# Performance work log

Measured on AMD Instinct MI355X. Metric: run time of the kernel, lower is better.

## Reference

```python
import jax, jax.numpy as jnp
import numpy as np

B, T, D = 1, 1024, 4096
H, HK, DH = 32, 8, 128          # n_heads, n_kv_heads, head_dim
N_REP = H // HK                 # GQA repeat factor
RQ, RKV, RO, RFF = 64, 64, 1024, 1024
INTER = 14336
EPS = 1e-5
THETA = 10000.0


def _rms_norm(x, w):
    # LLaMA RMSNorm: x * rsqrt(mean(x^2)+eps) * w
    var = jnp.mean(x * x, axis=-1, keepdims=True)
    return x * jax.lax.rsqrt(var + EPS) * w


def _rope_cos_sin(t_len, dh):
    # _SimpleRoPE semantics: interleaved repeat of angles (repeat_interleave(2))
    evens = jnp.arange(0, dh, 2, dtype=jnp.float32)
    inv = 1.0 / (THETA ** (evens / dh))                 # [dh/2]
    t = jnp.arange(t_len, dtype=jnp.float32)
    ang = t[:, None] * inv[None, :]                     # [T, dh/2]
    ang = jnp.repeat(ang, 2, axis=-1)                   # [T, dh]
    return jnp.cos(ang), jnp.sin(ang)


def _rotate_half(x):
    # HF rotate_half: split in half along last dim
    half = x.shape[-1] // 2
    return jnp.concatenate([-x[..., half:], x[..., :half]], axis=-1)


def _apply_rope(q, k, cos, sin):
    # q,k: [B,H,T,dh]; cos/sin: [T,dh] broadcast over B,H
    c = cos[None, None]
    s = sin[None, None]
    return q * c + _rotate_half(q) * s, k * c + _rotate_half(k) * s


def _proj_per_head(x, Us, V):
    # x: [B,T,D], V: [h,r,D], Us: [h,dh,r] -> [B,h,T,dh]
    xr = jnp.einsum('btd,hrd->bthr', x, V)
    return jnp.einsum('bthr,hdr->bhtd', xr, Us)


def setup_inputs() -> dict:
    key = jax.random.key(0)
    ks = jax.random.split(key, 16)
    sc = 0.02
    inp = {
        'hidden_states': jax.random.normal(ks[0], (B, T, D), jnp.float32),
        'ln1_w': jnp.ones((D,), jnp.float32),
        'ln2_w': jnp.ones((D,), jnp.float32),
        'q_Us': jax.random.normal(ks[1], (H, DH, RQ), jnp.float32) * sc,
        'q_V': jax.random.normal(ks[2], (H, RQ, D), jnp.float32) * sc,
        'k_Us': jax.random.normal(ks[3], (HK, DH, RKV), jnp.float32) * sc,
        'k_V': jax.random.normal(ks[4], (HK, RKV, D), jnp.float32) * sc,
        'v_Us': jax.random.normal(ks[5], (HK, DH, RKV), jnp.float32) * sc,
        'v_V': jax.random.normal(ks[6], (HK, RKV, D), jnp.float32) * sc,
        'o_Us': jax.random.normal(ks[7], (D, RO), jnp.float32) * sc,
        'o_V': jax.random.normal(ks[8], (RO, H * DH), jnp.float32) * sc,
        'g_Us': jax.random.normal(ks[9], (INTER, RFF), jnp.float32) * sc,
        'g_V': jax.random.normal(ks[10], (RFF, D), jnp.float32) * sc,
        'u_Us': jax.random.normal(ks[11], (INTER, RFF), jnp.float32) * sc,
        'u_V': jax.random.normal(ks[12], (RFF, D), jnp.float32) * sc,
        'd_Us': jax.random.normal(ks[13], (D, RFF), jnp.float32) * sc,
        'd_V': jax.random.normal(ks[14], (RFF, INTER), jnp.float32) * sc,
    }
    return inp


def reference(hidden_states, ln1_w, ln2_w, q_Us, q_V, k_Us, k_V, v_Us, v_V,
              o_Us, o_V, g_Us, g_V, u_Us, u_V, d_Us, d_V):
    x = hidden_states
    # --- attention ---
    h1 = _rms_norm(x, ln1_w)
    q = _proj_per_head(h1, q_Us, q_V)            # [B,H,T,dh]
    k = _proj_per_head(h1, k_Us, k_V)            # [B,HK,T,dh]
    v = _proj_per_head(h1, v_Us, v_V)            # [B,HK,T,dh]
    cos, sin = _rope_cos_sin(T, DH)
    q, k = _apply_rope(q, k, cos, sin)
    k = jnp.repeat(k, N_REP, axis=1)             # GQA expand -> [B,H,T,dh]
    v = jnp.repeat(v, N_REP, axis=1)
    scale = 1.0 / np.sqrt(DH)
    scores = jnp.einsum('bhtd,bhsd->bhts', q, k) * scale   # [B,H,T,T]
    causal = jnp.tril(jnp.ones((T, T), bool))
    scores = jnp.where(causal[None, None], scores, jnp.float32(-1e30))
    p = jax.nn.softmax(scores, axis=-1)
    attn = jnp.einsum('bhts,bhsd->bhtd', p, v)   # [B,H,T,dh]
    attn = attn.transpose(0, 2, 1, 3).reshape(B, T, H * DH)
    # low-rank o: y = attn @ W_o^T = (attn @ V^T) @ Us^T
    y = jnp.einsum('btr,dr->btd', jnp.einsum('bte,re->btr', attn, o_V), o_Us)
    x = x + y
    # --- SwiGLU MLP with low-rank factors ---
    h2 = _rms_norm(x, ln2_w)
    g = jnp.einsum('btr,ir->bti', jnp.einsum('btd,rd->btr', h2, g_V), g_Us)
    u = jnp.einsum('btr,ir->bti', jnp.einsum('btd,rd->btr', h2, u_V), u_Us)
    hmid = jax.nn.silu(g) * u                    # [B,T,INTER]
    dn = jnp.einsum('btr,dr->btd', jnp.einsum('bti,ri->btr', hmid, d_V), d_Us)
    return x + dn
```

## Files before the change

kernel.cpp:

```cpp
#include <hip/hip_runtime.h>
#include <math.h>


typedef __bf16 bf16;
typedef __bf16 bf16x8 __attribute__((ext_vector_type(8)));
typedef __bf16 bf16x4 __attribute__((ext_vector_type(4)));
typedef float  f32x4  __attribute__((ext_vector_type(4)));

#define EPI_BF16   0
#define EPI_BF16T  1
#define EPI_F32ADD 2
#define EPI_SILU1  3
#define EPI_MUL    4
#define EPI_PART   5

__device__ __forceinline__ void gld16(const void* g, void* l) {
    __builtin_amdgcn_global_load_lds(
        (const __attribute__((address_space(1))) unsigned int*)g,
        (__attribute__((address_space(3))) unsigned int*)l, 16, 0, 0);
}

template<int EPI>
__global__ __launch_bounds__(256)
void gemm3(const bf16* __restrict__ A, int lda, long sA,
           const bf16* __restrict__ B, int ldb, long sB, const bf16* __restrict__ B2,
           void* __restrict__ Cv, int ldc, long sC,
           const float* __restrict__ R, int Kc, int nsplit, int gx)
{
    __shared__ __align__(16) bf16 As[128 * 64];
    __shared__ __align__(16) bf16 Bs[128 * 64];

    const int tid = threadIdx.x, lane = tid & 63, w = tid >> 6;
    const int wr = w >> 1, wc = w & 1;

    int id = blockIdx.x;
    {
        const int nwg = gridDim.x;
        int q = nwg >> 3, rr = nwg & 7;
        int xcd = id & 7, off = id >> 3;
        id = (xcd < rr ? xcd * (q + 1) : rr * (q + 1) + (xcd - rr) * q) + off;
    }
    const int bm = id % gx, bn = id / gx, bz = blockIdx.z;
    const int ks = bz % nsplit, zb = bz / nsplit;

    const bf16* Bp = (B2 != nullptr && zb != 0) ? B2 : B;
    const bf16* Ab = A  + (long)zb * sA + (long)(bm * 128) * lda + (long)ks * Kc;
    const bf16* Bb = Bp + (long)zb * sB + (long)(bn * 128) * ldb + (long)ks * Kc;

    const int g = lane >> 4, r = lane & 15;
    f32x4 acc[4][4] = {};
    const int nt = Kc >> 6;

    for (int t = 0; t < nt; t++) {
        if (t) __syncthreads();
        const bf16* At = Ab + t * 64;
        const bf16* Bt = Bb + t * 64;
        #pragma unroll
        for (int i = 0; i < 4; i++) {
            int cb = w * 256 + i * 64, ci = cb + lane;
            int row = ci >> 3, col = ((ci & 7) ^ (row & 7)) * 8;
            gld16(At + (long)row * lda + col, &As[cb * 8]);
            gld16(Bt + (long)row * ldb + col, &Bs[cb * 8]);
        }
        __syncthreads();
        #pragma unroll
        for (int kk = 0; kk < 2; kk++) {
            bf16x8 af[4], bfr[4];
            #pragma unroll
            for (int m = 0; m < 4; m++) {
                int row = wr * 64 + m * 16 + r;
                af[m] = *(const bf16x8*)&As[row * 64 + (((kk * 4 + g) ^ (row & 7)) * 8)];
            }
            #pragma unroll
            for (int n = 0; n < 4; n++) {
                int row = wc * 64 + n * 16 + r;
                bfr[n] = *(const bf16x8*)&Bs[row * 64 + (((kk * 4 + g) ^ (row & 7)) * 8)];
            }
            #pragma unroll
            for (int m = 0; m < 4; m++)
                #pragma unroll
                for (int n = 0; n < 4; n++)
                    acc[m][n] = __builtin_amdgcn_mfma_f32_16x16x32_bf16(af[m], bfr[n], acc[m][n], 0, 0, 0);
        }
    }

    #pragma unroll
    for (int m = 0; m < 4; m++) {
        #pragma unroll
        for (int n = 0; n < 4; n++) {
            const int row0 = bm * 128 + wr * 64 + m * 16 + g * 4;
            const int col  = bn * 128 + wc * 64 + n * 16 + r;
            #pragma unroll
            for (int j = 0; j < 4; j++) {
                float v = acc[m][n][j];
                long row = row0 + j;
                if constexpr (EPI == EPI_BF16) {
                    ((bf16*)Cv)[(long)zb * sC + row * (long)ldc + col] = (bf16)v;
                } else if constexpr (EPI == EPI_BF16T) {
                    ((bf16*)Cv)[(long)zb * sC + (long)col * ldc + row] = (bf16)v;
                } else if constexpr (EPI == EPI_F32ADD) {
                    long idx = row * (long)ldc + col;
                    ((float*)Cv)[idx] = v + R[idx];
                } else if constexpr (EPI == EPI_PART) {
                    ((float*)Cv)[(long)bz * sC + row * (long)ldc + col] = v;
                } else if constexpr (EPI == EPI_SILU1) {
                    ((bf16*)Cv)[row * (long)ldc + col] = (bf16)(v / (1.f + __expf(-v)));
                } else {
                    bf16* p = &((bf16*)Cv)[row * (long)ldc + col];
                    *p = (bf16)((float)*p * v);
                }
            }
        }
    }
}

template<int EPI>
__global__ __launch_bounds__(256)
void gemm2(const bf16* __restrict__ A, int lda, long sA,
           const float* __restrict__ B, int ldb, long sB, const float* __restrict__ B2,
           void* __restrict__ Cv, int ldc, long sC,
           const float* __restrict__ R, int Kc, int nsplit)
{
    __shared__ __align__(16) bf16 As[2][128 * 64];
    __shared__ __align__(16) bf16 Bs[2][128 * 64];

    const int tid = threadIdx.x, lane = tid & 63, w = tid >> 6;
    const int wr = w >> 1, wc = w & 1;
    const int bm = blockIdx.x, bn = blockIdx.y, bz = blockIdx.z;
    const int ks = bz % nsplit, zb = bz / nsplit;

    const float* Bp = (B2 != nullptr && zb != 0) ? B2 : B;
    const bf16*  Ab = A  + (long)zb * sA + (long)(bm * 128) * lda + (long)ks * Kc;
    const float* Bb = Bp + (long)zb * sB + (long)(bn * 128) * ldb + (long)ks * Kc;

    const int g = lane >> 4, r = lane & 15;
    f32x4 acc[4][4] = {};
    const int nt = Kc >> 6;
    int cur = 0;

    {
        #pragma unroll
        for (int i = 0; i < 4; i++) {
            int cb = i * 256 + w * 64, ci = cb + lane;
            int arow = ci >> 3, acol = ((ci & 7) ^ (arow & 7)) * 8;
            gld16(Ab + (long)arow * lda + acol, &As[0][cb * 8]);
        }
        float4 fb[8];
        #pragma unroll
        for (int i = 0; i < 8; i++) {
            int p = i * 256 + tid;
            fb[i] = *(const float4*)(Bb + (long)(p >> 4) * ldb + (p & 15) * 4);
        }
        #pragma unroll
        for (int i = 0; i < 8; i++) {
            int p = i * 256 + tid, brow = p >> 4, c4 = p & 15;
            bf16x4 h = {(bf16)fb[i].x, (bf16)fb[i].y, (bf16)fb[i].z, (bf16)fb[i].w};
            *(bf16x4*)&Bs[0][brow * 64 + (((c4 >> 1) ^ (brow & 7)) * 8) + (c4 & 1) * 4] = h;
        }
    }
    __syncthreads();

    for (int t = 0; t < nt; t++) {
        float4 fb[8];
        if (t + 1 < nt) {
            const bf16* An = Ab + (t + 1) * 64;
            #pragma unroll
            for (int i = 0; i < 4; i++) {
                int cb = i * 256 + w * 64, ci = cb + lane;
                int arow = ci >> 3, acol = ((ci & 7) ^ (arow & 7)) * 8;
                gld16(An + (long)arow * lda + acol, &As[cur ^ 1][cb * 8]);
            }
            const float* Bn = Bb + (t + 1) * 64;
            #pragma unroll
            for (int i = 0; i < 8; i++) {
                int p = i * 256 + tid;
                fb[i] = *(const float4*)(Bn + (long)(p >> 4) * ldb + (p & 15) * 4);
            }
        }
        #pragma unroll
        for (int kk = 0; kk < 2; kk++) {
            bf16x8 af[4], bfr[4];
            #pragma unroll
            for (int m = 0; m < 4; m++) {
                int row = wr * 64 + m * 16 + r;
                af[m] = *(const bf16x8*)&As[cur][row * 64 + (((kk * 4 + g) ^ (row & 7)) * 8)];
            }
            #pragma unroll
            for (int n = 0; n < 4; n++) {
                int row = wc * 64 + n * 16 + r;
                bfr[n] = *(const bf16x8*)&Bs[cur][row * 64 + (((kk * 4 + g) ^ (row & 7)) * 8)];
            }
            #pragma unroll
            for (int m = 0; m < 4; m++)
                #pragma unroll
                for (int n = 0; n < 4; n++)
                    acc[m][n] = __builtin_amdgcn_mfma_f32_16x16x32_bf16(af[m], bfr[n], acc[m][n], 0, 0, 0);
        }
        if (t + 1 < nt) {
            #pragma unroll
            for (int i = 0; i < 8; i++) {
                int p = i * 256 + tid, brow = p >> 4, c4 = p & 15;
                bf16x4 h = {(bf16)fb[i].x, (bf16)fb[i].y, (bf16)fb[i].z, (bf16)fb[i].w};
                *(bf16x4*)&Bs[cur ^ 1][brow * 64 + (((c4 >> 1) ^ (brow & 7)) * 8) + (c4 & 1) * 4] = h;
            }
            __syncthreads();
            cur ^= 1;
        }
    }

    #pragma unroll
    for (int m = 0; m < 4; m++) {
        #pragma unroll
        for (int n = 0; n < 4; n++) {
            const int row0 = bm * 128 + wr * 64 + m * 16 + g * 4;
            const int col  = bn * 128 + wc * 64 + n * 16 + r;
            #pragma unroll
            for (int j = 0; j < 4; j++) {
                float v = acc[m][n][j];
                long row = row0 + j;
                if constexpr (EPI == EPI_BF16) {
                    ((bf16*)Cv)[(long)zb * sC + row * (long)ldc + col] = (bf16)v;
                } else if constexpr (EPI == EPI_BF16T) {
                    ((bf16*)Cv)[(long)zb * sC + (long)col * ldc + row] = (bf16)v;
                } else if constexpr (EPI == EPI_F32ADD) {
                    long idx = row * (long)ldc + col;
                    ((float*)Cv)[idx] = v + R[idx];
                } else if constexpr (EPI == EPI_PART) {
                    ((float*)Cv)[(long)bz * sC + row * (long)ldc + col] = v;
                } else if constexpr (EPI == EPI_SILU1) {
                    ((bf16*)Cv)[row * (long)ldc + col] = (bf16)(v / (1.f + __expf(-v)));
                } else {
                    bf16* p = &((bf16*)Cv)[row * (long)ldc + col];
                    *p = (bf16)((float)*p * v);
                }
            }
        }
    }
}

struct CvtArgs { const float* s[14]; bf16* d[14]; int n[14]; };

__global__ __launch_bounds__(256)
void cvt_k(CvtArgs a)
{
    const long stride = (long)gridDim.x * 256;
    #pragma unroll 1
    for (int ti = 0; ti < 14; ti++) {
        const float* __restrict__ s = a.s[ti];
        bf16* __restrict__ d = a.d[ti];
        long n8 = (long)a.n[ti] >> 3;
        for (long i = (long)blockIdx.x * 256 + threadIdx.x; i < n8; i += stride) {
            const float4* sp = (const float4*)s + i * 2;
            float4 f0 = sp[0], f1 = sp[1];
            bf16x8 h = {(bf16)f0.x,(bf16)f0.y,(bf16)f0.z,(bf16)f0.w,
                        (bf16)f1.x,(bf16)f1.y,(bf16)f1.z,(bf16)f1.w};
            *(bf16x8*)(d + i * 8) = h;
        }
    }
}

__global__ __launch_bounds__(256)
void reduce_k(const float* __restrict__ part, long pe, int np, bf16* __restrict__ out)
{
    long i = ((long)blockIdx.x * 256 + threadIdx.x) * 4;
    float4 s = *(const float4*)&part[i];
    for (int p = 1; p < np; p++) {
        float4 v = *(const float4*)&part[(long)p * pe + i];
        s.x += v.x; s.y += v.y; s.z += v.z; s.w += v.w;
    }
    bf16x4 o = {(bf16)s.x, (bf16)s.y, (bf16)s.z, (bf16)s.w};
    *(bf16x4*)&out[i] = o;
}

__global__ __launch_bounds__(256)
void rmsnorm_k(const float* __restrict__ x, const float* __restrict__ w,
               bf16* __restrict__ out)
{
    const int D = 4096;
    const long row = blockIdx.x;
    const float* xr = x + row * D;
    float4 v[4];
    float ss = 0.f;
    #pragma unroll
    for (int k = 0; k < 4; k++) {
        v[k] = *(const float4*)&xr[threadIdx.x * 4 + k * 1024];
        ss += v[k].x * v[k].x + v[k].y * v[k].y + v[k].z * v[k].z + v[k].w * v[k].w;
    }
    #pragma unroll
    for (int o = 32; o > 0; o >>= 1) ss += __shfl_down(ss, o);
    __shared__ float red[4];
    if ((threadIdx.x & 63) == 0) red[threadIdx.x >> 6] = ss;
    __syncthreads();
    float rs = rsqrtf((red[0] + red[1] + red[2] + red[3]) / D + 1e-5f);
    #pragma unroll
    for (int k = 0; k < 4; k++) {
        int i = threadIdx.x * 4 + k * 1024;
        float4 wv = *(const float4*)&w[i];
        bf16x4 o4 = {(bf16)(v[k].x * rs * wv.x), (bf16)(v[k].y * rs * wv.y),
                     (bf16)(v[k].z * rs * wv.z), (bf16)(v[k].w * rs * wv.w)};
        *(bf16x4*)&out[row * D + i] = o4;
    }
}

__global__ __launch_bounds__(256)
void rope_table_k(float* cs, float* sn)
{
    int idx = blockIdx.x * blockDim.x + threadIdx.x;
    int t = idx >> 6, i = idx & 63;
    float inv = powf(10000.0f, -(2.0f * i) / 128.0f);
    float a = (float)t * inv;
    cs[idx] = cosf(a);
    sn[idx] = sinf(a);
}

__global__ __launch_bounds__(256)
void rope_k(bf16* qk, const float* __restrict__ cs, const float* __restrict__ sn)
{
    long idx = (long)blockIdx.x * blockDim.x + threadIdx.x;
    int d = idx & 63;
    long ht = idx >> 6;
    int t = (int)(ht & 1023);
    bf16* p = qk + ht * 128;
    float x1 = (float)p[d], x2 = (float)p[d + 64];
    int i1 = d >> 1;
    float c1 = cs[t * 64 + i1],      s1 = sn[t * 64 + i1];
    float c2 = cs[t * 64 + 32 + i1], s2 = sn[t * 64 + 32 + i1];
    p[d]      = (bf16)(x1 * c1 - x2 * s1);
    p[d + 64] = (bf16)(x2 * c2 + x1 * s2);
}

__global__ __launch_bounds__(256)
void attn_k(const bf16* __restrict__ Q,
            const bf16* __restrict__ Kb,
            const bf16* __restrict__ Vt,
            bf16* __restrict__ O)
{
    const int T = 1024;
    __shared__ __align__(16) bf16 Ks[64][128];
    __shared__ __align__(16) bf16 Vs[128][64];
    __shared__ __align__(16) bf16 Ps[4][16][72];

    const int qt = blockIdx.x, h = blockIdx.y, hk = h >> 2;
    const int tid = threadIdx.x, lane = tid & 63, w = tid >> 6;
    const int g = lane >> 4, r = lane & 15;
    const int qrow0 = qt * 64 + w * 16;

    bf16x8 qf[4];
    const bf16* qp = Q + ((long)h * T + qrow0 + r) * 128;
    #pragma unroll
    for (int dc = 0; dc < 4; dc++) qf[dc] = *(const bf16x8*)(qp + dc * 32 + g * 8);

    f32x4 o_acc[8] = {};
    float m_run[4], l_run[4];
    #pragma unroll
    for (int j = 0; j < 4; j++) { m_run[j] = -1e30f; l_run[j] = 0.f; }

    const float scale = 0.08838834764831845f;
    const int kv_end = qt * 64 + 64;

    for (int kv0 = 0; kv0 < kv_end; kv0 += 64) {
        __syncthreads();
        {
            int tr = tid >> 2;
            const bf16* src = Kb + ((long)hk * T + kv0 + tr) * 128;
            #pragma unroll
            for (int q4 = 0; q4 < 4; q4++) {
                int c = (tid & 3) * 4 + q4;
                bf16x8 v = *(const bf16x8*)(src + c * 8);
                *(bf16x8*)&Ks[tr][(c ^ (tr & 7)) * 8] = v;
            }
        }
        {
            int dd = tid >> 1;
            const bf16* src = Vt + ((long)hk * 128 + dd) * T + kv0;
            #pragma unroll
            for (int q4 = 0; q4 < 4; q4++) {
                int c = (tid & 1) * 4 + q4;
                bf16x8 v = *(const bf16x8*)(src + c * 8);
                *(bf16x8*)&Vs[dd][(c ^ (dd & 7)) * 8] = v;
            }
        }
        __syncthreads();

        f32x4 s[4] = {};
        #pragma unroll
        for (int n = 0; n < 4; n++) {
            int tr = n * 16 + r;
            #pragma unroll
            for (int dc = 0; dc < 4; dc++) {
                int c = (dc * 4 + g) ^ (tr & 7);
                bf16x8 kf = *(const bf16x8*)&Ks[tr][c * 8];
                s[n] = __builtin_amdgcn_mfma_f32_16x16x32_bf16(qf[dc], kf, s[n], 0, 0, 0);
            }
        }

        #pragma unroll
        for (int j = 0; j < 4; j++) {
            int qpos = qrow0 + g * 4 + j;
            float mx = m_run[j];
            #pragma unroll
            for (int n = 0; n < 4; n++) {
                int kpos = kv0 + n * 16 + r;
                float sv = s[n][j] * scale;
                sv = (kpos <= qpos) ? sv : -1e30f;
                s[n][j] = sv;
                mx = fmaxf(mx, sv);
            }
            #pragma unroll
            for (int mask = 1; mask < 16; mask <<= 1) mx = fmaxf(mx, __shfl_xor(mx, mask));
            float corr = __expf(m_run[j] - mx);
            l_run[j] *= corr;
            #pragma unroll
            for (int db = 0; db < 8; db++) o_acc[db][j] *= corr;
            float ls = 0.f;
            #pragma unroll
            for (int n = 0; n < 4; n++) {
                float p = __expf(s[n][j] - mx);
                s[n][j] = p;
                ls += p;
            }
            #pragma unroll
            for (int mask = 1; mask < 16; mask <<= 1) ls += __shfl_xor(ls, mask);
            l_run[j] += ls;
            m_run[j] = mx;
        }

        #pragma unroll
        for (int n = 0; n < 4; n++)
            #pragma unroll
            for (int j = 0; j < 4; j++)
                Ps[w][g * 4 + j][n * 16 + r] = (bf16)s[n][j];
        __syncthreads();

        bf16x8 pf[2];
        #pragma unroll
        for (int kc = 0; kc < 2; kc++)
            pf[kc] = *(const bf16x8*)&Ps[w][r][kc * 32 + g * 8];
        #pragma unroll
        for (int db = 0; db < 8; db++) {
            #pragma unroll
            for (int kc = 0; kc < 2; kc++) {
                int dd = db * 16 + r;
                int c = (kc * 4 + g) ^ (dd & 7);
                bf16x8 vf = *(const bf16x8*)&Vs[dd][c * 8];
                o_acc[db] = __builtin_amdgcn_mfma_f32_16x16x32_bf16(pf[kc], vf, o_acc[db], 0, 0, 0);
            }
        }
    }

    #pragma unroll
    for (int db = 0; db < 8; db++) {
        #pragma unroll
        for (int j = 0; j < 4; j++) {
            int t = qrow0 + g * 4 + j;
            float v = o_acc[db][j] / l_run[j];
            O[(long)t * 4096 + h * 128 + db * 16 + r] = (bf16)v;
        }
    }
}

extern "C" void kernel_launch(void* const* d_in, const int* in_sizes, int n_in,
                              void* d_out, int out_size, void* d_ws, size_t ws_size,
                              hipStream_t stream)
{
    const float* X   = (const float*)d_in[0];
    const float* LN1 = (const float*)d_in[1];
    const float* LN2 = (const float*)d_in[2];
    const float* qUs = (const float*)d_in[3];
    const float* qV  = (const float*)d_in[4];
    const float* kUs = (const float*)d_in[5];
    const float* kV  = (const float*)d_in[6];
    const float* vUs = (const float*)d_in[7];
    const float* vV  = (const float*)d_in[8];
    const float* oUs = (const float*)d_in[9];
    const float* oV  = (const float*)d_in[10];
    const float* gUs = (const float*)d_in[11];
    const float* gV  = (const float*)d_in[12];
    const float* uUs = (const float*)d_in[13];
    const float* uV  = (const float*)d_in[14];
    const float* dUs = (const float*)d_in[15];
    const float* dV  = (const float*)d_in[16];
    float* OUT = (float*)d_out;

    char* w = (char*)d_ws;
    bf16*  h1   = (bf16*)(w + 0);
    bf16*  xrq  = (bf16*)(w + 8388608);
    bf16*  xrk  = (bf16*)(w + 12582912);
    bf16*  xrv  = (bf16*)(w + 13631488);
    bf16*  qb   = (bf16*)(w + 14680064);
    bf16*  kb   = (bf16*)(w + 23068672);
    bf16*  vt   = (bf16*)(w + 25165824);
    float* cs   = (float*)(w + 27262976);
    float* sn   = (float*)(w + 27525120);
    bf16*  att  = (bf16*)(w + 27787264);
    bf16*  r1   = (bf16*)(w + 36175872);
    bf16*  h2   = (bf16*)(w + 0);
    bf16*  gr   = (bf16*)(w + 8388608);
    bf16*  ur   = (bf16*)(w + 10485760);
    bf16*  hmid = (bf16*)(w + 12582912);
    bf16*  dr   = (bf16*)(w + 41943040);
    const size_t ARENA  = 44040192;
    const size_t PARTSZ = 33554432;
    float* part = (float*)(w + ARENA);

    bf16* wa = (bf16*)(w + ARENA + PARTSZ);
    const long N_qUs = 262144,  N_qV = 8388608, N_kUs = 65536,  N_kV = 2097152;
    const long N_vUs = 65536,   N_vV = 2097152, N_oUs = 4194304,N_oV = 4194304;
    const long N_gUs = 14680064,N_gV = 4194304, N_uUs = 14680064,N_uV = 4194304;
    const long N_dUs = 4194304, N_dV = 14680064;
    long off = 0;
    bf16* qUsb = wa + off; off += N_qUs;  bf16* qVb = wa + off; off += N_qV;
    bf16* kUsb = wa + off; off += N_kUs;  bf16* kVb = wa + off; off += N_kV;
    bf16* vUsb = wa + off; off += N_vUs;  bf16* vVb = wa + off; off += N_vV;
    bf16* oUsb = wa + off; off += N_oUs;  bf16* oVb = wa + off; off += N_oV;
    bf16* gUsb = wa + off; off += N_gUs;  bf16* gVb = wa + off; off += N_gV;
    bf16* uUsb = wa + off; off += N_uUs;  bf16* uVb = wa + off; off += N_uV;
    bf16* dUsb = wa + off; off += N_dUs;  bf16* dVb = wa + off; off += N_dV;

    const bool med = ws_size >= ARENA + PARTSZ;
    const bool big = ws_size >= ARENA + PARTSZ + (size_t)off * 2;

    dim3 blk(256);

    if (big) {
        CvtArgs ca;
        ca.s[0]=qUs; ca.d[0]=qUsb; ca.n[0]=(int)N_qUs;
        ca.s[1]=qV;  ca.d[1]=qVb;  ca.n[1]=(int)N_qV;
        ca.s[2]=kUs; ca.d[2]=kUsb; ca.n[2]=(int)N_kUs;
        ca.s[3]=kV;  ca.d[3]=kVb;  ca.n[3]=(int)N_kV;
        ca.s[4]=vUs; ca.d[4]=vUsb; ca.n[4]=(int)N_vUs;
        ca.s[5]=vV;  ca.d[5]=vVb;  ca.n[5]=(int)N_vV;
        ca.s[6]=oUs; ca.d[6]=oUsb; ca.n[6]=(int)N_oUs;
        ca.s[7]=oV;  ca.d[7]=oVb;  ca.n[7]=(int)N_oV;
        ca.s[8]=gUs; ca.d[8]=gUsb; ca.n[8]=(int)N_gUs;
        ca.s[9]=gV;  ca.d[9]=gVb;  ca.n[9]=(int)N_gV;
        ca.s[10]=uUs;ca.d[10]=uUsb;ca.n[10]=(int)N_uUs;
        ca.s[11]=uV; ca.d[11]=uVb; ca.n[11]=(int)N_uV;
        ca.s[12]=dUs;ca.d[12]=dUsb;ca.n[12]=(int)N_dUs;
        ca.s[13]=dV; ca.d[13]=dVb; ca.n[13]=(int)N_dV;
        cvt_k<<<2048, blk, 0, stream>>>(ca);

        rmsnorm_k<<<1024, blk, 0, stream>>>(X, LN1, h1);
        gemm3<EPI_PART><<<dim3(128,1,4), blk, 0, stream>>>(h1,4096,0, qVb,4096,0,nullptr, part,2048,2097152, nullptr, 1024,4, 8);
        reduce_k<<<2048, blk, 0, stream>>>(part, 2097152, 4, xrq);
        gemm3<EPI_PART><<<dim3(32,1,8), blk, 0, stream>>>(h1,4096,0, kVb,4096,0,vVb, part,512,524288, nullptr, 1024,4, 8);
        reduce_k<<<512, blk, 0, stream>>>(part,             524288, 4, xrk);
        reduce_k<<<512, blk, 0, stream>>>(part + 4L*524288, 524288, 4, xrv);

        gemm3<EPI_BF16 ><<<dim3(8,1,32), blk, 0, stream>>>(xrq,2048,64, qUsb,64,8192,nullptr, qb,128,131072, nullptr, 64,1, 8);
        gemm3<EPI_BF16 ><<<dim3(8,1, 8), blk, 0, stream>>>(xrk, 512,64, kUsb,64,8192,nullptr, kb,128,131072, nullptr, 64,1, 8);
        gemm3<EPI_BF16T><<<dim3(8,1, 8), blk, 0, stream>>>(xrv, 512,64, vUsb,64,8192,nullptr, vt,1024,131072, nullptr, 64,1, 8);
        rope_table_k<<<256, blk, 0, stream>>>(cs, sn);
        rope_k<<<8192, blk, 0, stream>>>(qb, cs, sn);
        rope_k<<<2048, blk, 0, stream>>>(kb, cs, sn);
        attn_k<<<dim3(16,32), blk, 0, stream>>>(qb, kb, vt, att);

        gemm3<EPI_PART><<<dim3(64,1,4), blk, 0, stream>>>(att,4096,0, oVb,4096,0,nullptr, part,1024,1048576, nullptr, 1024,4, 8);
        reduce_k<<<1024, blk, 0, stream>>>(part, 1048576, 4, r1);
        gemm3<EPI_F32ADD><<<dim3(256,1,1), blk, 0, stream>>>(r1,1024,0, oUsb,1024,0,nullptr, OUT,4096,0, X, 1024,1, 8);

        rmsnorm_k<<<1024, blk, 0, stream>>>(OUT, LN2, h2);
        gemm3<EPI_PART><<<dim3(64,1,8), blk, 0, stream>>>(h2,4096,0, gVb,4096,0,uVb, part,1024,1048576, nullptr, 1024,4, 8);
        reduce_k<<<1024, blk, 0, stream>>>(part,              1048576, 4, gr);
        reduce_k<<<1024, blk, 0, stream>>>(part + 4L*1048576, 1048576, 4, ur);
        gemm3<EPI_SILU1><<<dim3(896,1,1), blk, 0, stream>>>(gr,1024,0, gUsb,1024,0,nullptr, hmid,14336,0, nullptr, 1024,1, 8);
        gemm3<EPI_MUL  ><<<dim3(896,1,1), blk, 0, stream>>>(ur,1024,0, uUsb,1024,0,nullptr, hmid,14336,0, nullptr, 1024,1, 8);
        gemm3<EPI_PART><<<dim3(64,1,7), blk, 0, stream>>>(hmid,14336,0, dVb,14336,0,nullptr, part,1024,1048576, nullptr, 2048,7, 8);
        reduce_k<<<1024, blk, 0, stream>>>(part, 1048576, 7, dr);
        gemm3<EPI_F32ADD><<<dim3(256,1,1), blk, 0, stream>>>(dr,1024,0, dUsb,1024,0,nullptr, OUT,4096,0, OUT, 1024,1, 8);
        return;
    }

    rmsnorm_k<<<1024, blk, 0, stream>>>(X, LN1, h1);
    if (med) {
        gemm2<EPI_PART><<<dim3(8,16,4), blk, 0, stream>>>(h1,4096,0, qV,4096,0,nullptr, part,2048,2097152, nullptr, 1024, 4);
        reduce_k<<<2048, blk, 0, stream>>>(part, 2097152, 4, xrq);
        gemm2<EPI_PART><<<dim3(8,4,8), blk, 0, stream>>>(h1,4096,0, kV,4096,0,vV, part,512,524288, nullptr, 1024, 4);
        reduce_k<<<512, blk, 0, stream>>>(part,             524288, 4, xrk);
        reduce_k<<<512, blk, 0, stream>>>(part + 4L*524288, 524288, 4, xrv);
    } else {
        gemm2<EPI_BF16><<<dim3(8,16,1), blk, 0, stream>>>(h1,4096,0, qV,4096,0,nullptr, xrq,2048,0, nullptr, 4096, 1);
        gemm2<EPI_BF16><<<dim3(8, 4,1), blk, 0, stream>>>(h1,4096,0, kV,4096,0,nullptr, xrk, 512,0, nullptr, 4096, 1);
        gemm2<EPI_BF16><<<dim3(8, 4,1), blk, 0, stream>>>(h1,4096,0, vV,4096,0,nullptr, xrv, 512,0, nullptr, 4096, 1);
    }
    gemm2<EPI_BF16 ><<<dim3(8,1,32), blk, 0, stream>>>(xrq,2048,64, qUs,64,8192,nullptr, qb,128,131072, nullptr, 64, 1);
    gemm2<EPI_BF16 ><<<dim3(8,1, 8), blk, 0, stream>>>(xrk, 512,64, kUs,64,8192,nullptr, kb,128,131072, nullptr, 64, 1);
    gemm2<EPI_BF16T><<<dim3(8,1, 8), blk, 0, stream>>>(xrv, 512,64, vUs,64,8192,nullptr, vt,1024,131072, nullptr, 64, 1);
    rope_table_k<<<256, blk, 0, stream>>>(cs, sn);
    rope_k<<<8192, blk, 0, stream>>>(qb, cs, sn);
    rope_k<<<2048, blk, 0, stream>>>(kb, cs, sn);
    attn_k<<<dim3(16,32), blk, 0, stream>>>(qb, kb, vt, att);
    if (med) {
        gemm2<EPI_PART><<<dim3(8,8,4), blk, 0, stream>>>(att,4096,0, oV,4096,0,nullptr, part,1024,1048576, nullptr, 1024, 4);
        reduce_k<<<1024, blk, 0, stream>>>(part, 1048576, 4, r1);
    } else {
        gemm2<EPI_BF16><<<dim3(8,8,1), blk, 0, stream>>>(att,4096,0, oV,4096,0,nullptr, r1,1024,0, nullptr, 4096, 1);
    }
    gemm2<EPI_F32ADD><<<dim3(8,32,1), blk, 0, stream>>>(r1,1024,0, oUs,1024,0,nullptr, OUT,4096,0, X, 1024, 1);
    rmsnorm_k<<<1024, blk, 0, stream>>>(OUT, LN2, h2);
    if (med) {
        gemm2<EPI_PART><<<dim3(8,8,8), blk, 0, stream>>>(h2,4096,0, gV,4096,0,uV, part,1024,1048576, nullptr, 1024, 4);
        reduce_k<<<1024, blk, 0, stream>>>(part,              1048576, 4, gr);
        reduce_k<<<1024, blk, 0, stream>>>(part + 4L*1048576, 1048576, 4, ur);
    } else {
        gemm2<EPI_BF16><<<dim3(8,8,1), blk, 0, stream>>>(h2,4096,0, gV,4096,0,nullptr, gr,1024,0, nullptr, 4096, 1);
        gemm2<EPI_BF16><<<dim3(8,8,1), blk, 0, stream>>>(h2,4096,0, uV,4096,0,nullptr, ur,1024,0, nullptr, 4096, 1);
    }
    gemm2<EPI_SILU1><<<dim3(8,112,1), blk, 0, stream>>>(gr,1024,0, gUs,1024,0,nullptr, hmid,14336,0, nullptr, 1024, 1);
    gemm2<EPI_MUL  ><<<dim3(8,112,1), blk, 0, stream>>>(ur,1024,0, uUs,1024,0,nullptr, hmid,14336,0, nullptr, 1024, 1);
    if (med) {
        gemm2<EPI_PART><<<dim3(8,8,7), blk, 0, stream>>>(hmid,14336,0, dV,14336,0,nullptr, part,1024,1048576, nullptr, 2048, 7);
        reduce_k<<<1024, blk, 0, stream>>>(part, 1048576, 7, dr);
    } else {
        gemm2<EPI_BF16><<<dim3(8,8,1), blk, 0, stream>>>(hmid,14336,0, dV,14336,0,nullptr, dr,1024,0, nullptr, 14336, 1);
    }
    gemm2<EPI_F32ADD><<<dim3(8,32,1), blk, 0, stream>>>(dr,1024,0, dUs,1024,0,nullptr, OUT,4096,0, OUT, 1024, 1);
}
```

Before: 570.9 us.

## Load fp32 weights directly in GEMM and drop separate bf16 conversion pass

Replaces the upfront kernel that converted all fp32 weight matrices to bf16 with a GEMM variant that stages the fp32 B operand directly into shared memory and converts to bf16 when building MFMA fragments. This removes a full read-plus-write pass over roughly 90M weight elements each call. In exchange, each GEMM reads twice as many bytes for B and uses double the shared memory for the B tile, which may lower occupancy. The fast path now runs whenever the partial-sum workspace is available, rather than requiring the larger bf16 weight arena.

```diff
diff --git a/kernel.cpp b/kernel.cpp
--- a/kernel.cpp
+++ b/kernel.cpp
@@ -22,13 +22,13 @@
 
 template<int EPI>
 __global__ __launch_bounds__(256)
-void gemm3(const bf16* __restrict__ A, int lda, long sA,
-           const bf16* __restrict__ B, int ldb, long sB, const bf16* __restrict__ B2,
-           void* __restrict__ Cv, int ldc, long sC,
-           const float* __restrict__ R, int Kc, int nsplit, int gx)
-{
-    __shared__ __align__(16) bf16 As[128 * 64];
-    __shared__ __align__(16) bf16 Bs[128 * 64];
+void gemm3f(const bf16* __restrict__ A, int lda, long sA,
+            const float* __restrict__ B, int ldb, long sB, const float* __restrict__ B2,
+            void* __restrict__ Cv, int ldc, long sC,
+            const float* __restrict__ R, int Kc, int nsplit, int gx)
+{
+    __shared__ __align__(16) bf16  As[128 * 64];
+    __shared__ __align__(16) float Bs[128 * 64];
 
     const int tid = threadIdx.x, lane = tid & 63, w = tid >> 6;
     const int wr = w >> 1, wc = w & 1;
@@ -43,9 +43,9 @@
     const int bm = id % gx, bn = id / gx, bz = blockIdx.z;
     const int ks = bz % nsplit, zb = bz / nsplit;
 
-    const bf16* Bp = (B2 != nullptr && zb != 0) ? B2 : B;
-    const bf16* Ab = A  + (long)zb * sA + (long)(bm * 128) * lda + (long)ks * Kc;
-    const bf16* Bb = Bp + (long)zb * sB + (long)(bn * 128) * ldb + (long)ks * Kc;
+    const float* Bp = (B2 != nullptr && zb != 0) ? B2 : B;
+    const bf16*  Ab = A  + (long)zb * sA + (long)(bm * 128) * lda + (long)ks * Kc;
+    const float* Bb = Bp + (long)zb * sB + (long)(bn * 128) * ldb + (long)ks * Kc;
 
     const int g = lane >> 4, r = lane & 15;
     f32x4 acc[4][4] = {};
@@ -53,14 +53,19 @@
 
     for (int t = 0; t < nt; t++) {
         if (t) __syncthreads();
-        const bf16* At = Ab + t * 64;
-        const bf16* Bt = Bb + t * 64;
+        const bf16*  At = Ab + t * 64;
+        const float* Bt = Bb + t * 64;
         #pragma unroll
         for (int i = 0; i < 4; i++) {
             int cb = w * 256 + i * 64, ci = cb + lane;
             int row = ci >> 3, col = ((ci & 7) ^ (row & 7)) * 8;
             gld16(At + (long)row * lda + col, &As[cb * 8]);
-            gld16(Bt + (long)row * ldb + col, &Bs[cb * 8]);
+        }
+        #pragma unroll
+        for (int i = 0; i < 8; i++) {
+            int cb = w * 512 + i * 64, ci = cb + lane;
+            int row = ci >> 4, col = ((ci & 15) ^ (row & 15)) * 4;
+            gld16(Bt + (long)row * ldb + col, &Bs[cb * 4]);
         }
         __syncthreads();
         #pragma unroll
@@ -74,7 +79,11 @@
             #pragma unroll
             for (int n = 0; n < 4; n++) {
                 int row = wc * 64 + n * 16 + r;
-                bfr[n] = *(const bf16x8*)&Bs[row * 64 + (((kk * 4 + g) ^ (row & 7)) * 8)];
+                int c0 = kk * 8 + g * 2;
+                f32x4 lo = *(const f32x4*)&Bs[row * 64 + (((c0    ) ^ (row & 15)) * 4)];
+                f32x4 hi = *(const f32x4*)&Bs[row * 64 + (((c0 + 1) ^ (row & 15)) * 4)];
+                bfr[n] = bf16x8{(bf16)lo[0], (bf16)lo[1], (bf16)lo[2], (bf16)lo[3],
+                                (bf16)hi[0], (bf16)hi[1], (bf16)hi[2], (bf16)hi[3]};
             }
             #pragma unroll
             for (int m = 0; m < 4; m++)
@@ -234,27 +243,6 @@
                     *p = (bf16)((float)*p * v);
                 }
             }
-        }
-    }
-}
-
-struct CvtArgs { const float* s[14]; bf16* d[14]; int n[14]; };
-
-__global__ __launch_bounds__(256)
-void cvt_k(CvtArgs a)
-{
-    const long stride = (long)gridDim.x * 256;
-    #pragma unroll 1
-    for (int ti = 0; ti < 14; ti++) {
-        const float* __restrict__ s = a.s[ti];
-        bf16* __restrict__ d = a.d[ti];
-        long n8 = (long)a.n[ti] >> 3;
-        for (long i = (long)blockIdx.x * 256 + threadIdx.x; i < n8; i += stride) {
-            const float4* sp = (const float4*)s + i * 2;
-            float4 f0 = sp[0], f1 = sp[1];
-            bf16x8 h = {(bf16)f0.x,(bf16)f0.y,(bf16)f0.z,(bf16)f0.w,
-                        (bf16)f1.x,(bf16)f1.y,(bf16)f1.z,(bf16)f1.w};
-            *(bf16x8*)(d + i * 8) = h;
         }
     }
 }
@@ -502,87 +490,46 @@
     const size_t ARENA  = 44040192;
     const size_t PARTSZ = 33554432;
     float* part = (float*)(w + ARENA);
-
-    bf16* wa = (bf16*)(w + ARENA + PARTSZ);
-    const long N_qUs = 262144,  N_qV = 8388608, N_kUs = 65536,  N_kV = 2097152;
-    const long N_vUs = 65536,   N_vV = 2097152, N_oUs = 4194304,N_oV = 4194304;
-    const long N_gUs = 14680064,N_gV = 4194304, N_uUs = 14680064,N_uV = 4194304;
-    const long N_dUs = 4194304, N_dV = 14680064;
-    long off = 0;
-    bf16* qUsb = wa + off; off += N_qUs;  bf16* qVb = wa + off; off += N_qV;
-    bf16* kUsb = wa + off; off += N_kUs;  bf16* kVb = wa + off; off += N_kV;
-    bf16* vUsb = wa + off; off += N_vUs;  bf16* vVb = wa + off; off += N_vV;
-    bf16* oUsb = wa + off; off += N_oUs;  bf16* oVb = wa + off; off += N_oV;
-    bf16* gUsb = wa + off; off += N_gUs;  bf16* gVb = wa + off; off += N_gV;
-    bf16* uUsb = wa + off; off += N_uUs;  bf16* uVb = wa + off; off += N_uV;
-    bf16* dUsb = wa + off; off += N_dUs;  bf16* dVb = wa + off; off += N_dV;
-
     const bool med = ws_size >= ARENA + PARTSZ;
-    const bool big = ws_size >= ARENA + PARTSZ + (size_t)off * 2;
 
     dim3 blk(256);
 
-    if (big) {
-        CvtArgs ca;
-        ca.s[0]=qUs; ca.d[0]=qUsb; ca.n[0]=(int)N_qUs;
-        ca.s[1]=qV;  ca.d[1]=qVb;  ca.n[1]=(int)N_qV;
-        ca.s[2]=kUs; ca.d[2]=kUsb; ca.n[2]=(int)N_kUs;
-        ca.s[3]=kV;  ca.d[3]=kVb;  ca.n[3]=(int)N_kV;
-        ca.s[4]=vUs; ca.d[4]=vUsb; ca.n[4]=(int)N_vUs;
-        ca.s[5]=vV;  ca.d[5]=vVb;  ca.n[5]=(int)N_vV;
-        ca.s[6]=oUs; ca.d[6]=oUsb; ca.n[6]=(int)N_oUs;
-        ca.s[7]=oV;  ca.d[7]=oVb;  ca.n[7]=(int)N_oV;
-        ca.s[8]=gUs; ca.d[8]=gUsb; ca.n[8]=(int)N_gUs;
-        ca.s[9]=gV;  ca.d[9]=gVb;  ca.n[9]=(int)N_gV;
-        ca.s[10]=uUs;ca.d[10]=uUsb;ca.n[10]=(int)N_uUs;
-        ca.s[11]=uV; ca.d[11]=uVb; ca.n[11]=(int)N_uV;
-        ca.s[12]=dUs;ca.d[12]=dUsb;ca.n[12]=(int)N_dUs;
-        ca.s[13]=dV; ca.d[13]=dVb; ca.n[13]=(int)N_dV;
-        cvt_k<<<2048, blk, 0, stream>>>(ca);
-
+    if (med) {
         rmsnorm_k<<<1024, blk, 0, stream>>>(X, LN1, h1);
-        gemm3<EPI_PART><<<dim3(128,1,4), blk, 0, stream>>>(h1,4096,0, qVb,4096,0,nullptr, part,2048,2097152, nullptr, 1024,4, 8);
+        gemm3f<EPI_PART><<<dim3(128,1,4), blk, 0, stream>>>(h1,4096,0, qV,4096,0,nullptr, part,2048,2097152, nullptr, 1024,4, 8);
         reduce_k<<<2048, blk, 0, stream>>>(part, 2097152, 4, xrq);
-        gemm3<EPI_PART><<<dim3(32,1,8), blk, 0, stream>>>(h1,4096,0, kVb,4096,0,vVb, part,512,524288, nullptr, 1024,4, 8);
+        gemm3f<EPI_PART><<<dim3(32,1,8), blk, 0, stream>>>(h1,4096,0, kV,4096,0,vV, part,512,524288, nullptr, 1024,4, 8);
         reduce_k<<<512, blk, 0, stream>>>(part,             524288, 4, xrk);
         reduce_k<<<512, blk, 0, stream>>>(part + 4L*524288, 524288, 4, xrv);
 
-        gemm3<EPI_BF16 ><<<dim3(8,1,32), blk, 0, stream>>>(xrq,2048,64, qUsb,64,8192,nullptr, qb,128,131072, nullptr, 64,1, 8);
-        gemm3<EPI_BF16 ><<<dim3(8,1, 8), blk, 0, stream>>>(xrk, 512,64, kUsb,64,8192,nullptr, kb,128,131072, nullptr, 64,1, 8);
-        gemm3<EPI_BF16T><<<dim3(8,1, 8), blk, 0, stream>>>(xrv, 512,64, vUsb,64,8192,nullptr, vt,1024,131072, nullptr, 64,1, 8);
+        gemm3f<EPI_BF16 ><<<dim3(8,1,32), blk, 0, stream>>>(xrq,2048,64, qUs,64,8192,nullptr, qb,128,131072, nullptr, 64,1, 8);
+        gemm3f<EPI_BF16 ><<<dim3(8,1, 8), blk, 0, stream>>>(xrk, 512,64, kUs,64,8192,nullptr, kb,128,131072, nullptr, 64,1, 8);
+        gemm3f<EPI_BF16T><<<dim3(8,1, 8), blk, 0, stream>>>(xrv, 512,64, vUs,64,8192,nullptr, vt,1024,131072, nullptr, 64,1, 8);
         rope_table_k<<<256, blk, 0, stream>>>(cs, sn);
         rope_k<<<8192, blk, 0, stream>>>(qb, cs, sn);
         rope_k<<<2048, blk, 0, stream>>>(kb, cs, sn);
         attn_k<<<dim3(16,32), blk, 0, stream>>>(qb, kb, vt, att);
 
-        gemm3<EPI_PART><<<dim3(64,1,4), blk, 0, stream>>>(att,4096,0, oVb,4096,0,nullptr, part,1024,1048576, nullptr, 1024,4, 8);
+        gemm3f<EPI_PART><<<dim3(64,1,4), blk, 0, stream>>>(att,4096,0, oV,4096,0,nullptr, part,1024,1048576, nullptr, 1024,4, 8);
         reduce_k<<<1024, blk, 0, stream>>>(part, 1048576, 4, r1);
-        gemm3<EPI_F32ADD><<<dim3(256,1,1), blk, 0, stream>>>(r1,1024,0, oUsb,1024,0,nullptr, OUT,4096,0, X, 1024,1, 8);
+        gemm3f<EPI_F32ADD><<<dim3(256,1,1), blk, 0, stream>>>(r1,1024,0, oUs,1024,0,nullptr, OUT,4096,0, X, 1024,1, 8);
 
         rmsnorm_k<<<1024, blk, 0, stream>>>(OUT, LN2, h2);
-        gemm3<EPI_PART><<<dim3(64,1,8), blk, 0, stream>>>(h2,4096,0, gVb,4096,0,uVb, part,1024,1048576, nullptr, 1024,4, 8);
+        gemm3f<EPI_PART><<<dim3(64,1,8), blk, 0, stream>>>(h2,4096,0, gV,4096,0,uV, part,1024,1048576, nullptr, 1024,4, 8);
         reduce_k<<<1024, blk, 0, stream>>>(part,              1048576, 4, gr);
         reduce_k<<<1024, blk, 0, stream>>>(part + 4L*1048576, 1048576, 4, ur);
-        gemm3<EPI_SILU1><<<dim3(896,1,1), blk, 0, stream>>>(gr,1024,0, gUsb,1024,0,nullptr, hmid,14336,0, nullptr, 1024,1, 8);
-        gemm3<EPI_MUL  ><<<dim3(896,1,1), blk, 0, stream>>>(ur,1024,0, uUsb,1024,0,nullptr, hmid,14336,0, nullptr, 1024,1, 8);
-        gemm3<EPI_PART><<<dim3(64,1,7), blk, 0, stream>>>(hmid,14336,0, dVb,14336,0,nullptr, part,1024,1048576, nullptr, 2048,7, 8);
+        gemm3f<EPI_SILU1><<<dim3(896,1,1), blk, 0, stream>>>(gr,1024,0, gUs,1024,0,nullptr, hmid,14336,0, nullptr, 1024,1, 8);
+        gemm3f<EPI_MUL  ><<<dim3(896,1,1), blk, 0, stream>>>(ur,1024,0, uUs,1024,0,nullptr, hmid,14336,0, nullptr, 1024,1, 8);
+        gemm3f<EPI_PART><<<dim3(64,1,7), blk, 0, stream>>>(hmid,14336,0, dV,14336,0,nullptr, part,1024,1048576, nullptr, 2048,7, 8);
         reduce_k<<<1024, blk, 0, stream>>>(part, 1048576, 7, dr);
-        gemm3<EPI_F32ADD><<<dim3(256,1,1), blk, 0, stream>>>(dr,1024,0, dUsb,1024,0,nullptr, OUT,4096,0, OUT, 1024,1, 8);
+        gemm3f<EPI_F32ADD><<<dim3(256,1,1), blk, 0, stream>>>(dr,1024,0, dUs,1024,0,nullptr, OUT,4096,0, OUT, 1024,1, 8);
         return;
     }
 
     rmsnorm_k<<<1024, blk, 0, stream>>>(X, LN1, h1);
-    if (med) {
-        gemm2<EPI_PART><<<dim3(8,16,4), blk, 0, stream>>>(h1,4096,0, qV,4096,0,nullptr, part,2048,2097152, nullptr, 1024, 4);
-        reduce_k<<<2048, blk, 0, stream>>>(part, 2097152, 4, xrq);
-        gemm2<EPI_PART><<<dim3(8,4,8), blk, 0, stream>>>(h1,4096,0, kV,4096,0,vV, part,512,524288, nullptr, 1024, 4);
-        reduce_k<<<512, blk, 0, stream>>>(part,             524288, 4, xrk);
-        reduce_k<<<512, blk, 0, stream>>>(part + 4L*524288, 524288, 4, xrv);
-    } else {
-        gemm2<EPI_BF16><<<dim3(8,16,1), blk, 0, stream>>>(h1,4096,0, qV,4096,0,nullptr, xrq,2048,0, nullptr, 4096, 1);
-        gemm2<EPI_BF16><<<dim3(8, 4,1), blk, 0, stream>>>(h1,4096,0, kV,4096,0,nullptr, xrk, 512,0, nullptr, 4096, 1);
-        gemm2<EPI_BF16><<<dim3(8, 4,1), blk, 0, stream>>>(h1,4096,0, vV,4096,0,nullptr, xrv, 512,0, nullptr, 4096, 1);
-    }
+    gemm2<EPI_BF16><<<dim3(8,16,1), blk, 0, stream>>>(h1,4096,0, qV,4096,0,nullptr, xrq,2048,0, nullptr, 4096, 1);
+    gemm2<EPI_BF16><<<dim3(8, 4,1), blk, 0, stream>>>(h1,4096,0, kV,4096,0,nullptr, xrk, 512,0, nullptr, 4096, 1);
+    gemm2<EPI_BF16><<<dim3(8, 4,1), blk, 0, stream>>>(h1,4096,0, vV,4096,0,nullptr, xrv, 512,0, nullptr, 4096, 1);
     gemm2<EPI_BF16 ><<<dim3(8,1,32), blk, 0, stream>>>(xrq,2048,64, qUs,64,8192,nullptr, qb,128,131072, nullptr, 64, 1);
     gemm2<EPI_BF16 ><<<dim3(8,1, 8), blk, 0, stream>>>(xrk, 512,64, kUs,64,8192,nullptr, kb,128,131072, nullptr, 64, 1);
     gemm2<EPI_BF16T><<<dim3(8,1, 8), blk, 0, stream>>>(xrv, 512,64, vUs,64,8192,nullptr, vt,1024,131072, nullptr, 64, 1);
@@ -590,29 +537,13 @@
     rope_k<<<8192, blk, 0, stream>>>(qb, cs, sn);
     rope_k<<<2048, blk, 0, stream>>>(kb, cs, sn);
     attn_k<<<dim3(16,32), blk, 0, stream>>>(qb, kb, vt, att);
-    if (med) {
-        gemm2<EPI_PART><<<dim3(8,8,4), blk, 0, stream>>>(att,4096,0, oV,4096,0,nullptr, part,1024,1048576, nullptr, 1024, 4);
-        reduce_k<<<1024, blk, 0, stream>>>(part, 1048576, 4, r1);
-    } else {
-        gemm2<EPI_BF16><<<dim3(8,8,1), blk, 0, stream>>>(att,4096,0, oV,4096,0,nullptr, r1,1024,0, nullptr, 4096, 1);
-    }
+    gemm2<EPI_BF16><<<dim3(8,8,1), blk, 0, stream>>>(att,4096,0, oV,4096,0,nullptr, r1,1024,0, nullptr, 4096, 1);
     gemm2<EPI_F32ADD><<<dim3(8,32,1), blk, 0, stream>>>(r1,1024,0, oUs,1024,0,nullptr, OUT,4096,0, X, 1024, 1);
     rmsnorm_k<<<1024, blk, 0, stream>>>(OUT, LN2, h2);
-    if (med) {
-        gemm2<EPI_PART><<<dim3(8,8,8), blk, 0, stream>>>(h2,4096,0, gV,4096,0,uV, part,1024,1048576, nullptr, 1024, 4);
-        reduce_k<<<1024, blk, 0, stream>>>(part,              1048576, 4, gr);
-        reduce_k<<<1024, blk, 0, stream>>>(part + 4L*1048576, 1048576, 4, ur);
-    } else {
-        gemm2<EPI_BF16><<<dim3(8,8,1), blk, 0, stream>>>(h2,4096,0, gV,4096,0,nullptr, gr,1024,0, nullptr, 4096, 1);
-        gemm2<EPI_BF16><<<dim3(8,8,1), blk, 0, stream>>>(h2,4096,0, uV,4096,0,nullptr, ur,1024,0, nullptr, 4096, 1);
-    }
+    gemm2<EPI_BF16><<<dim3(8,8,1), blk, 0, stream>>>(h2,4096,0, gV,4096,0,nullptr, gr,1024,0, nullptr, 4096, 1);
+    gemm2<EPI_BF16><<<dim3(8,8,1), blk, 0, stream>>>(h2,4096,0, uV,4096,0,nullptr, ur,1024,0, nullptr, 4096, 1);
     gemm2<EPI_SILU1><<<dim3(8,112,1), blk, 0, stream>>>(gr,1024,0, gUs,1024,0,nullptr, hmid,14336,0, nullptr, 1024, 1);
     gemm2<EPI_MUL  ><<<dim3(8,112,1), blk, 0, stream>>>(ur,1024,0, uUs,1024,0,nullptr, hmid,14336,0, nullptr, 1024, 1);
-    if (med) {
-        gemm2<EPI_PART><<<dim3(8,8,7), blk, 0, stream>>>(hmid,14336,0, dV,14336,0,nullptr, part,1024,1048576, nullptr, 2048, 7);
-        reduce_k<<<1024, blk, 0, stream>>>(part, 1048576, 7, dr);
-    } else {
-        gemm2<EPI_BF16><<<dim3(8,8,1), blk, 0, stream>>>(hmid,14336,0, dV,14336,0,nullptr, dr,1024,0, nullptr, 14336, 1);
-    }
+    gemm2<EPI_BF16><<<dim3(8,8,1), blk, 0, stream>>>(hmid,14336,0, dV,14336,0,nullptr, dr,1024,0, nullptr, 14336, 1);
     gemm2<EPI_F32ADD><<<dim3(8,32,1), blk, 0, stream>>>(dr,1024,0, dUs,1024,0,nullptr, OUT,4096,0, OUT, 1024, 1);
 }
```

After: 526.5 us. 7.8% less time.
